# Kernel tuning notes

Hardware: AMD Instinct MI355X
Metric: run time of the kernel (lower is better)

The kernel has to match this reference:

```python
import jax, jax.numpy as jnp
import numpy as np

NU, NI, E, D = 100000, 50000, 500000, 64
L = 3  # number of NGCF layers
SLOPE = 0.2
EPS = 1e-12


def setup_inputs() -> dict:
    key = jax.random.key(0)
    ks = jax.random.split(key, 12)
    scale = 1.0 / np.sqrt(D)  # roughly xavier-ish magnitude
    return {
        "feat_user": jax.random.normal(ks[0], (NU, D), jnp.float32) * scale,
        "feat_item": jax.random.normal(ks[1], (NI, D), jnp.float32) * scale,
        "W1": jax.random.normal(ks[2], (L, D, D), jnp.float32) * scale,
        "b1": jnp.zeros((L, D), jnp.float32),
        "W2": jax.random.normal(ks[3], (L, D, D), jnp.float32) * scale,
        "b2": jnp.zeros((L, D), jnp.float32),
        "u_idx": jax.random.randint(ks[4], (E,), 0, NU),
        "i_idx": jax.random.randint(ks[5], (E,), 0, NI),
        "users": jax.random.randint(ks[6], (8192,), 0, NU),
        "pos_items": jax.random.randint(ks[7], (8192,), 0, NI),
        "neg_items": jax.random.randint(ks[8], (8192,), 0, NI),
    }


def _l2norm(h):
    n = jnp.sqrt(jnp.sum(h * h, axis=1, keepdims=True))
    return h / jnp.maximum(n, EPS)


def reference(feat_user, feat_item, W1, b1, W2, b2, u_idx, i_idx, users, pos_items, neg_items):
    # symmetric edge norm 1/sqrt(deg_u * deg_i), same for both directions
    ones = jnp.ones((E,), jnp.float32)
    deg_u = jax.ops.segment_sum(ones, u_idx, num_segments=NU)
    deg_i = jax.ops.segment_sum(ones, i_idx, num_segments=NI)
    norm = (deg_u[u_idx] * deg_i[i_idx]) ** -0.5  # [E]
    norm = norm[:, None]

    hu, hi = feat_user, feat_item
    user_embeds, item_embeds = [hu], [hi]
    for l in range(L):
        w1, bb1, w2, bb2 = W1[l], b1[l], W2[l], b2[l]
        pu = hu @ w1 + bb1  # self-loop message W1(h) per user node
        pi = hi @ w1 + bb1
        eu = hu[u_idx]      # [E, D] gathered src features
        ei = hi[i_idx]
        pw = (eu * ei) @ w2 + bb2  # shared elementwise-product term
        m_u2i = norm * (pu[u_idx] + pw)  # user -> item messages
        m_i2u = norm * (pi[i_idx] + pw)  # item -> user messages
        hu = pu + jax.ops.segment_sum(m_i2u, u_idx, num_segments=NU)
        hi = pi + jax.ops.segment_sum(m_u2i, i_idx, num_segments=NI)
        hu = _l2norm(jax.nn.leaky_relu(hu, SLOPE))
        hi = _l2norm(jax.nn.leaky_relu(hi, SLOPE))
        user_embeds.append(hu)
        item_embeds.append(hi)

    user_embd = jnp.concatenate(user_embeds, axis=1)  # [NU, (L+1)*D]
    item_embd = jnp.concatenate(item_embeds, axis=1)
    return (user_embd[users], item_embd[pos_items], item_embd[neg_items])
```

## Files before the change

kernel.cpp:

```cpp
#include <hip/hip_runtime.h>

#define NU_N 100000
#define NI_N 50000
#define NN_N 150000
#define E_N  500000
#define NSEL 8192
#define GB   18750
#define OB   1536

typedef short s8v __attribute__((ext_vector_type(8)));
typedef short s4v __attribute__((ext_vector_type(4)));
typedef float f4v __attribute__((ext_vector_type(4)));

__device__ __forceinline__ float bf2f(unsigned short h) {
  union { unsigned u; float f; } v; v.u = ((unsigned)h) << 16; return v.f;
}
__device__ __forceinline__ unsigned short f2bf(float f) {
  union { float f; unsigned u; } v; v.f = f;
  unsigned u = v.u;
  u += 0x7FFFu + ((u >> 16) & 1u);
  return (unsigned short)(u >> 16);
}

__global__ void k_cvtW(const float* __restrict__ w1, const float* __restrict__ w2,
                       unsigned short* __restrict__ o1, unsigned short* __restrict__ o2) {
  int t = blockIdx.x * blockDim.x + threadIdx.x;
  if (t >= 3 * 8 * 64) return;
  int lane = t & 63;
  int fk = (t >> 6) & 7;
  int l = t >> 9;
  int n = fk >> 1, kh = fk & 1;
  int lm = lane & 15, lqq = lane >> 4;
  int dst = l * 4096 + (fk << 9) + (lane << 3);
  s8v v1, v2;
#pragma unroll
  for (int j = 0; j < 8; j++) {
    int src = l * 4096 + (32 * kh + 8 * lqq + j) * 64 + 16 * n + lm;
    v1[j] = (short)f2bf(w1[src]);
    v2[j] = (short)f2bf(w2[src]);
  }
  *(s8v*)(o1 + dst) = v1;
  *(s8v*)(o2 + dst) = v2;
}

__global__ void k_cvt8s(const float* __restrict__ fu, const float* __restrict__ fi,
                        unsigned short* __restrict__ h, unsigned short* __restrict__ hs,
                        const float* __restrict__ rdeg) {
  int t = blockIdx.x * blockDim.x + threadIdx.x;
  if (t >= NN_N * 8) return;
  int i = t * 8;
  int row = t >> 3;
  const float* src = row < NU_N ? (fu + i) : (fi + (i - NU_N * 64));
  float rw = rdeg[row];
  float4 a = *(const float4*)(src);
  float4 b = *(const float4*)(src + 4);
  s8v o, os;
  o[0] = (short)f2bf(a.x); os[0] = (short)f2bf(a.x * rw);
  o[1] = (short)f2bf(a.y); os[1] = (short)f2bf(a.y * rw);
  o[2] = (short)f2bf(a.z); os[2] = (short)f2bf(a.z * rw);
  o[3] = (short)f2bf(a.w); os[3] = (short)f2bf(a.w * rw);
  o[4] = (short)f2bf(b.x); os[4] = (short)f2bf(b.x * rw);
  o[5] = (short)f2bf(b.y); os[5] = (short)f2bf(b.y * rw);
  o[6] = (short)f2bf(b.z); os[6] = (short)f2bf(b.z * rw);
  o[7] = (short)f2bf(b.w); os[7] = (short)f2bf(b.w * rw);
  *(s8v*)(h + i) = o;
  *(s8v*)(hs + i) = os;
}

__global__ void k_build(const int* __restrict__ u_idx, const int* __restrict__ i_idx,
                        int* __restrict__ cnt,
                        unsigned short* __restrict__ nbrU, int* __restrict__ nbrI) {
  int t = blockIdx.x * blockDim.x + threadIdx.x;
  if (t >= E_N / 4) return;
  int e = t * 4;
  int4 uu = *(const int4*)(u_idx + e);
  int4 ii = *(const int4*)(i_idx + e);
  int u[4] = {uu.x, uu.y, uu.z, uu.w};
  int it[4] = {ii.x, ii.y, ii.z, ii.w};
  int su[4], si[4];
#pragma unroll
  for (int k = 0; k < 4; k++) su[k] = atomicAdd(cnt + u[k], 1);
#pragma unroll
  for (int k = 0; k < 4; k++) si[k] = atomicAdd(cnt + NU_N + it[k], 1);
#pragma unroll
  for (int k = 0; k < 4; k++) {
    if (su[k] < 32) nbrU[(u[k] << 5) + su[k]] = (unsigned short)it[k];
    if (si[k] < 64) nbrI[(it[k] << 6) + si[k]] = u[k];
  }
}

__global__ void k_meta(const int* __restrict__ cnt, float* __restrict__ rdeg) {
  int g = blockIdx.x * blockDim.x + threadIdx.x;
  if (g >= NN_N) return;
  int d = cnt[g];
  rdeg[g] = d > 0 ? 1.0f / sqrtf((float)d) : 0.0f;
}

__device__ __forceinline__ void out_body(int t, const float* __restrict__ fu,
                                         const float* __restrict__ fi,
                                         const unsigned short* __restrict__ h,
                                         const int* __restrict__ users,
                                         const int* __restrict__ pos,
                                         const int* __restrict__ neg,
                                         float* __restrict__ out, int l) {
  int j4 = (t & 15) * 4;
  int row = (t >> 4) & (NSEL - 1);
  int grp = t >> 17;
  int sr = grp == 0 ? users[row] : (grp == 1 ? pos[row] : neg[row]);
  float4 v;
  if (l == 0) {
    const float* f = grp == 0 ? fu : fi;
    v = *(const float4*)(f + (size_t)sr * 64 + j4);
  } else {
    const unsigned short* hh = h + (size_t)(grp == 0 ? sr : NU_N + sr) * 64 + j4;
    s4v x = *(const s4v*)hh;
    v.x = bf2f((unsigned short)x[0]); v.y = bf2f((unsigned short)x[1]);
    v.z = bf2f((unsigned short)x[2]); v.w = bf2f((unsigned short)x[3]);
  }
  *(float4*)(out + (size_t)grp * NSEL * 256 + (size_t)row * 256 + (size_t)l * 64 + j4) = v;
}

template <int CSUM>
__global__ void k_gather(const unsigned short* __restrict__ hs,
                         const int* __restrict__ cnt,
                         const unsigned short* __restrict__ nbrU, const int* __restrict__ nbrI,
                         const float* __restrict__ rdeg,
                         unsigned short* __restrict__ s, float* __restrict__ csum,
                         const float* __restrict__ fu, const float* __restrict__ fi,
                         const unsigned short* __restrict__ h,
                         const int* __restrict__ users, const int* __restrict__ pos,
                         const int* __restrict__ neg, float* __restrict__ out, int lslice) {
  if (blockIdx.x >= GB) {
    int t = (blockIdx.x - GB) * 256 + threadIdx.x;
    out_body(t, fu, fi, h, users, pos, neg, out, lslice);
    return;
  }
  int wv = (blockIdx.x * blockDim.x + threadIdx.x) >> 6;
  int lane = threadIdx.x & 63;
  int half = lane >> 5;
  int lane32 = lane & 31;
  int q = lane32 >> 3;
  int m = lane & 7;
  int g = wv * 2 + half;
  int d = cnt[g];
  bool isU = g < NU_N;
  int dcap = isU ? 32 : 64;
  d = d < dcap ? d : dcap;
  int k0 = isU ? (g << 5) : ((g - NU_N) << 6);
  int myid = NN_N;
  if (lane32 < d) myid = isU ? (NU_N + (int)nbrU[k0 + lane32]) : nbrI[k0 + lane32];
  float myw = 0.0f;
  if (CSUM) myw = rdeg[myid];
  float acc[8] = {0.f, 0.f, 0.f, 0.f, 0.f, 0.f, 0.f, 0.f};
  float c = 0.f;
  int dc = d < 32 ? d : 32;
  int nit = (dc + 15) >> 4;
  int nitA = __shfl(nit, 0), nitB = __shfl(nit, 32);
  int niter = nitA > nitB ? nitA : nitB;
  for (int i = 0; i < niter; i++) {
    int b0 = (half << 5) + (i << 4) + q;
    int n0 = __shfl(myid, b0);
    int n1 = __shfl(myid, b0 + 4);
    int n2 = __shfl(myid, b0 + 8);
    int n3 = __shfl(myid, b0 + 12);
    if (CSUM) {
      c += __shfl(myw, b0) + __shfl(myw, b0 + 4) +
           __shfl(myw, b0 + 8) + __shfl(myw, b0 + 12);
    }
    s8v v0 = *(const s8v*)(hs + (size_t)n0 * 64 + m * 8);
    s8v v1 = *(const s8v*)(hs + (size_t)n1 * 64 + m * 8);
    s8v v2 = *(const s8v*)(hs + (size_t)n2 * 64 + m * 8);
    s8v v3 = *(const s8v*)(hs + (size_t)n3 * 64 + m * 8);
#pragma unroll
    for (int j = 0; j < 8; j++)
      acc[j] += (bf2f((unsigned short)v0[j]) + bf2f((unsigned short)v1[j])) +
                (bf2f((unsigned short)v2[j]) + bf2f((unsigned short)v3[j]));
  }
  for (int t = 32 + q; t < d; t += 4) {
    int nb = nbrI[k0 + t];
    if (CSUM) c += rdeg[nb];
    s8v v = *(const s8v*)(hs + (size_t)nb * 64 + m * 8);
#pragma unroll
    for (int j = 0; j < 8; j++) acc[j] += bf2f((unsigned short)v[j]);
  }
#pragma unroll
  for (int off = 8; off <= 16; off <<= 1) {
#pragma unroll
    for (int j = 0; j < 8; j++) acc[j] += __shfl_xor(acc[j], off);
    if (CSUM) c += __shfl_xor(c, off);
  }
  float rw = rdeg[g];
  if (q == 0) {
    s8v ov;
#pragma unroll
    for (int j = 0; j < 8; j++) ov[j] = (short)f2bf(acc[j] * rw);
    *(s8v*)(s + (size_t)g * 64 + m * 8) = ov;
    if (CSUM && m == 0) csum[g] = c;
  }
}

__global__ void k_update(unsigned short* __restrict__ h, unsigned short* __restrict__ hs,
                         const unsigned short* __restrict__ s,
                         const float* __restrict__ csum, const float* __restrict__ rdeg,
                         const unsigned short* __restrict__ w1s, const unsigned short* __restrict__ w2s,
                         const float* __restrict__ b1, const float* __restrict__ b2) {
  int lane = threadIdx.x & 63;
  int lm = lane & 15, lq = lane >> 4;
  int tile = (blockIdx.x * blockDim.x + threadIdx.x) >> 6;
  if (tile >= NN_N / 16) return;
  s8v f1[4][2], f2w[4][2];
#pragma unroll
  for (int n = 0; n < 4; n++)
#pragma unroll
    for (int kh = 0; kh < 2; kh++) {
      int off = (((n << 1) | kh) << 9) + (lane << 3);
      f1[n][kh]  = *(const s8v*)(w1s + off);
      f2w[n][kh] = *(const s8v*)(w2s + off);
    }
  int m0 = tile << 4;
  size_t rowo = (size_t)(m0 + lm) * 64;
  s8v h0 = *(const s8v*)(h + rowo + 8 * lq);
  s8v h1 = *(const s8v*)(h + rowo + 32 + 8 * lq);
  s8v s0 = *(const s8v*)(s + rowo + 8 * lq);
  s8v s1 = *(const s8v*)(s + rowo + 32 + 8 * lq);
  s8v a10, a11, a20, a21;
#pragma unroll
  for (int j = 0; j < 8; j++) {
    float hv0 = bf2f((unsigned short)h0[j]), sv0 = bf2f((unsigned short)s0[j]);
    float hv1 = bf2f((unsigned short)h1[j]), sv1 = bf2f((unsigned short)s1[j]);
    a10[j] = (short)f2bf(hv0 + sv0); a20[j] = (short)f2bf(hv0 * sv0);
    a11[j] = (short)f2bf(hv1 + sv1); a21[j] = (short)f2bf(hv1 * sv1);
  }
  f4v c[4];
#pragma unroll
  for (int n = 0; n < 4; n++) c[n] = (f4v){0.f, 0.f, 0.f, 0.f};
#pragma unroll
  for (int n = 0; n < 4; n++) {
    c[n] = __builtin_amdgcn_mfma_f32_16x16x32_bf16(a10, f1[n][0], c[n], 0, 0, 0);
    c[n] = __builtin_amdgcn_mfma_f32_16x16x32_bf16(a11, f1[n][1], c[n], 0, 0, 0);
    c[n] = __builtin_amdgcn_mfma_f32_16x16x32_bf16(a20, f2w[n][0], c[n], 0, 0, 0);
    c[n] = __builtin_amdgcn_mfma_f32_16x16x32_bf16(a21, f2w[n][1], c[n], 0, 0, 0);
  }
  float b1c[4], b2c[4];
#pragma unroll
  for (int n = 0; n < 4; n++) { b1c[n] = b1[16 * n + lm]; b2c[n] = b2[16 * n + lm]; }
  float cm[4], rd[4];
#pragma unroll
  for (int r = 0; r < 4; r++) {
    int row = m0 + 4 * lq + r;
    rd[r] = rdeg[row];
    cm[r] = csum[row] * rd[r];
  }
  float x[4][4], ss[4] = {0.f, 0.f, 0.f, 0.f};
#pragma unroll
  for (int n = 0; n < 4; n++)
#pragma unroll
    for (int r = 0; r < 4; r++) {
      float v = c[n][r] + b1c[n] + cm[r] * (b1c[n] + b2c[n]);
      v = v > 0.0f ? v : 0.2f * v;
      x[n][r] = v;
      ss[r] += v * v;
    }
#pragma unroll
  for (int r = 0; r < 4; r++) {
#pragma unroll
    for (int off = 1; off < 16; off <<= 1) ss[r] += __shfl_xor(ss[r], off);
    ss[r] = 1.0f / fmaxf(sqrtf(ss[r]), 1e-12f);
  }
#pragma unroll
  for (int n = 0; n < 4; n++)
#pragma unroll
    for (int r = 0; r < 4; r++) {
      size_t o = (size_t)(m0 + 4 * lq + r) * 64 + 16 * n + lm;
      float hv = x[n][r] * ss[r];
      h[o]  = f2bf(hv);
      hs[o] = f2bf(hv * rd[r]);
    }
}

__global__ void k_out(const float* __restrict__ fu, const float* __restrict__ fi,
                      const unsigned short* __restrict__ h,
                      const int* __restrict__ users, const int* __restrict__ pos,
                      const int* __restrict__ neg, float* __restrict__ out, int l) {
  int t = blockIdx.x * blockDim.x + threadIdx.x;
  if (t >= 3 * NSEL * 16) return;
  out_body(t, fu, fi, h, users, pos, neg, out, l);
}

extern "C" void kernel_launch(void* const* d_in, const int* in_sizes, int n_in,
                              void* d_out, int out_size, void* d_ws, size_t ws_size,
                              hipStream_t stream) {
  (void)in_sizes; (void)n_in; (void)out_size; (void)ws_size;
  const float* fu = (const float*)d_in[0];
  const float* fi = (const float*)d_in[1];
  const float* W1 = (const float*)d_in[2];
  const float* b1 = (const float*)d_in[3];
  const float* W2 = (const float*)d_in[4];
  const float* b2 = (const float*)d_in[5];
  const int* u_idx = (const int*)d_in[6];
  const int* i_idx = (const int*)d_in[7];
  const int* users = (const int*)d_in[8];
  const int* pos   = (const int*)d_in[9];
  const int* neg   = (const int*)d_in[10];
  float* out = (float*)d_out;

  char* w = (char*)d_ws;
  auto alloc = [&](size_t bytes) { char* p = w; w += (bytes + 255) & ~(size_t)255; return p; };
  unsigned short* h  = (unsigned short*)alloc((size_t)NN_N * 64 * 2);
  unsigned short* hs = (unsigned short*)alloc((size_t)(NN_N + 1) * 64 * 2);
  unsigned short* sb = (unsigned short*)alloc((size_t)NN_N * 64 * 2);
  int*   cnt  = (int*)alloc((size_t)NN_N * 4);
  float* csum = (float*)alloc((size_t)NN_N * 4);
  float* rdeg = (float*)alloc((size_t)(NN_N + 1) * 4);
  unsigned short* nbrU = (unsigned short*)alloc((size_t)NU_N * 32 * 2);
  int*   nbrI = (int*)alloc((size_t)NI_N * 64 * 4);
  unsigned short* w1s = (unsigned short*)alloc((size_t)3 * 4096 * 2);
  unsigned short* w2s = (unsigned short*)alloc((size_t)3 * 4096 * 2);

  hipMemsetAsync(cnt, 0, (size_t)NN_N * 4, stream);
  hipMemsetAsync(hs + (size_t)NN_N * 64, 0, 128, stream);
  hipMemsetAsync(rdeg + NN_N, 0, 4, stream);
  k_build<<<(E_N / 4 + 255) / 256, 256, 0, stream>>>(u_idx, i_idx, cnt, nbrU, nbrI);
  k_meta<<<(NN_N + 255) / 256, 256, 0, stream>>>(cnt, rdeg);

  k_cvt8s<<<(NN_N * 8 + 255) / 256, 256, 0, stream>>>(fu, fi, h, hs, rdeg);
  k_cvtW<<<(3 * 8 * 64 + 255) / 256, 256, 0, stream>>>(W1, W2, w1s, w2s);

  for (int l = 0; l < 3; l++) {
    if (l == 0)
      k_gather<1><<<GB + OB, 256, 0, stream>>>(hs, cnt, nbrU, nbrI, rdeg, sb, csum,
                                               fu, fi, h, users, pos, neg, out, 0);
    else
      k_gather<0><<<GB + OB, 256, 0, stream>>>(hs, cnt, nbrU, nbrI, rdeg, sb, csum,
                                               fu, fi, h, users, pos, neg, out, l);
    k_update<<<((NN_N / 16) * 64 + 255) / 256, 256, 0, stream>>>(
        h, hs, sb, csum, rdeg, w1s + (size_t)l * 4096, w2s + (size_t)l * 4096,
        b1 + (size_t)l * 64, b2 + (size_t)l * 64);
  }
  k_out<<<(3 * NSEL * 16 + 255) / 256, 256, 0, stream>>>(fu, fi, h, users, pos, neg, out, 3);
}
```

Before: 228.3 us.

## Drop pre-scaled hs buffer, apply degree weights in gather, fuse init kernels

Removes the separate degree-prescaled bf16 feature copy (hs). The gather now reads h directly and multiplies each neighbour row by its rdeg weight, which it loads anyway. The edge-build, feature-conversion and weight-conversion kernels are merged into one launch. Feature conversion no longer waits for rdeg, so it can overlap with the atomic edge build. The aim is to cut the extra hs write in each update and at init, plus two kernel launches. The cost is extra multiplies in the gather and one fewer rounding step, which changes numerics slightly. The edge build also moves from four edges per thread to one.

```diff
diff --git a/kernel.cpp b/kernel.cpp
--- a/kernel.cpp
+++ b/kernel.cpp
@@ -7,6 +7,9 @@
 #define NSEL 8192
 #define GB   18750
 #define OB   1536
+#define BB   1954
+#define CB   4688
+#define WB   6
 
 typedef short s8v __attribute__((ext_vector_type(8)));
 typedef short s4v __attribute__((ext_vector_type(4)));
@@ -22,70 +25,57 @@
   return (unsigned short)(u >> 16);
 }
 
-__global__ void k_cvtW(const float* __restrict__ w1, const float* __restrict__ w2,
+__global__ void k_init(const int* __restrict__ u_idx, const int* __restrict__ i_idx,
+                       int* __restrict__ cnt,
+                       unsigned short* __restrict__ nbrU, int* __restrict__ nbrI,
+                       const float* __restrict__ fu, const float* __restrict__ fi,
+                       unsigned short* __restrict__ h,
+                       const float* __restrict__ w1, const float* __restrict__ w2,
                        unsigned short* __restrict__ o1, unsigned short* __restrict__ o2) {
-  int t = blockIdx.x * blockDim.x + threadIdx.x;
-  if (t >= 3 * 8 * 64) return;
-  int lane = t & 63;
-  int fk = (t >> 6) & 7;
-  int l = t >> 9;
-  int n = fk >> 1, kh = fk & 1;
-  int lm = lane & 15, lqq = lane >> 4;
-  int dst = l * 4096 + (fk << 9) + (lane << 3);
-  s8v v1, v2;
-#pragma unroll
-  for (int j = 0; j < 8; j++) {
-    int src = l * 4096 + (32 * kh + 8 * lqq + j) * 64 + 16 * n + lm;
-    v1[j] = (short)f2bf(w1[src]);
-    v2[j] = (short)f2bf(w2[src]);
-  }
-  *(s8v*)(o1 + dst) = v1;
-  *(s8v*)(o2 + dst) = v2;
-}
-
-__global__ void k_cvt8s(const float* __restrict__ fu, const float* __restrict__ fi,
-                        unsigned short* __restrict__ h, unsigned short* __restrict__ hs,
-                        const float* __restrict__ rdeg) {
-  int t = blockIdx.x * blockDim.x + threadIdx.x;
-  if (t >= NN_N * 8) return;
-  int i = t * 8;
-  int row = t >> 3;
-  const float* src = row < NU_N ? (fu + i) : (fi + (i - NU_N * 64));
-  float rw = rdeg[row];
-  float4 a = *(const float4*)(src);
-  float4 b = *(const float4*)(src + 4);
-  s8v o, os;
-  o[0] = (short)f2bf(a.x); os[0] = (short)f2bf(a.x * rw);
-  o[1] = (short)f2bf(a.y); os[1] = (short)f2bf(a.y * rw);
-  o[2] = (short)f2bf(a.z); os[2] = (short)f2bf(a.z * rw);
-  o[3] = (short)f2bf(a.w); os[3] = (short)f2bf(a.w * rw);
-  o[4] = (short)f2bf(b.x); os[4] = (short)f2bf(b.x * rw);
-  o[5] = (short)f2bf(b.y); os[5] = (short)f2bf(b.y * rw);
-  o[6] = (short)f2bf(b.z); os[6] = (short)f2bf(b.z * rw);
-  o[7] = (short)f2bf(b.w); os[7] = (short)f2bf(b.w * rw);
-  *(s8v*)(h + i) = o;
-  *(s8v*)(hs + i) = os;
-}
-
-__global__ void k_build(const int* __restrict__ u_idx, const int* __restrict__ i_idx,
-                        int* __restrict__ cnt,
-                        unsigned short* __restrict__ nbrU, int* __restrict__ nbrI) {
-  int t = blockIdx.x * blockDim.x + threadIdx.x;
-  if (t >= E_N / 4) return;
-  int e = t * 4;
-  int4 uu = *(const int4*)(u_idx + e);
-  int4 ii = *(const int4*)(i_idx + e);
-  int u[4] = {uu.x, uu.y, uu.z, uu.w};
-  int it[4] = {ii.x, ii.y, ii.z, ii.w};
-  int su[4], si[4];
-#pragma unroll
-  for (int k = 0; k < 4; k++) su[k] = atomicAdd(cnt + u[k], 1);
-#pragma unroll
-  for (int k = 0; k < 4; k++) si[k] = atomicAdd(cnt + NU_N + it[k], 1);
-#pragma unroll
-  for (int k = 0; k < 4; k++) {
-    if (su[k] < 32) nbrU[(u[k] << 5) + su[k]] = (unsigned short)it[k];
-    if (si[k] < 64) nbrI[(it[k] << 6) + si[k]] = u[k];
+  int b = blockIdx.x;
+  if (b < BB) {
+    int e = b * 256 + threadIdx.x;
+    if (e >= E_N) return;
+    int u = u_idx[e], it = i_idx[e];
+    int su = atomicAdd(cnt + u, 1);
+    if (su < 32) nbrU[(u << 5) + su] = (unsigned short)it;
+    int si = atomicAdd(cnt + NU_N + it, 1);
+    if (si < 64) nbrI[(it << 6) + si] = u;
+    return;
+  }
+  if (b < BB + CB) {
+    int t = (b - BB) * 256 + threadIdx.x;
+    if (t >= NN_N * 8) return;
+    int i = t * 8;
+    const float* src = i < NU_N * 64 ? (fu + i) : (fi + (i - NU_N * 64));
+    float4 a = *(const float4*)(src);
+    float4 bb = *(const float4*)(src + 4);
+    s8v o;
+    o[0] = (short)f2bf(a.x);  o[1] = (short)f2bf(a.y);
+    o[2] = (short)f2bf(a.z);  o[3] = (short)f2bf(a.w);
+    o[4] = (short)f2bf(bb.x); o[5] = (short)f2bf(bb.y);
+    o[6] = (short)f2bf(bb.z); o[7] = (short)f2bf(bb.w);
+    *(s8v*)(h + i) = o;
+    return;
+  }
+  {
+    int t = (b - BB - CB) * 256 + threadIdx.x;
+    if (t >= 3 * 8 * 64) return;
+    int lane = t & 63;
+    int fk = (t >> 6) & 7;
+    int l = t >> 9;
+    int n = fk >> 1, kh = fk & 1;
+    int lm = lane & 15, lqq = lane >> 4;
+    int dst = l * 4096 + (fk << 9) + (lane << 3);
+    s8v v1, v2;
+#pragma unroll
+    for (int j = 0; j < 8; j++) {
+      int src = l * 4096 + (32 * kh + 8 * lqq + j) * 64 + 16 * n + lm;
+      v1[j] = (short)f2bf(w1[src]);
+      v2[j] = (short)f2bf(w2[src]);
+    }
+    *(s8v*)(o1 + dst) = v1;
+    *(s8v*)(o2 + dst) = v2;
   }
 }
 
@@ -121,13 +111,12 @@
 }
 
 template <int CSUM>
-__global__ void k_gather(const unsigned short* __restrict__ hs,
+__global__ void k_gather(const unsigned short* __restrict__ h,
                          const int* __restrict__ cnt,
                          const unsigned short* __restrict__ nbrU, const int* __restrict__ nbrI,
                          const float* __restrict__ rdeg,
                          unsigned short* __restrict__ s, float* __restrict__ csum,
                          const float* __restrict__ fu, const float* __restrict__ fi,
-                         const unsigned short* __restrict__ h,
                          const int* __restrict__ users, const int* __restrict__ pos,
                          const int* __restrict__ neg, float* __restrict__ out, int lslice) {
   if (blockIdx.x >= GB) {
@@ -149,8 +138,7 @@
   int k0 = isU ? (g << 5) : ((g - NU_N) << 6);
   int myid = NN_N;
   if (lane32 < d) myid = isU ? (NU_N + (int)nbrU[k0 + lane32]) : nbrI[k0 + lane32];
-  float myw = 0.0f;
-  if (CSUM) myw = rdeg[myid];
+  float myw = rdeg[myid];
   float acc[8] = {0.f, 0.f, 0.f, 0.f, 0.f, 0.f, 0.f, 0.f};
   float c = 0.f;
   int dc = d < 32 ? d : 32;
@@ -163,25 +151,27 @@
     int n1 = __shfl(myid, b0 + 4);
     int n2 = __shfl(myid, b0 + 8);
     int n3 = __shfl(myid, b0 + 12);
-    if (CSUM) {
-      c += __shfl(myw, b0) + __shfl(myw, b0 + 4) +
-           __shfl(myw, b0 + 8) + __shfl(myw, b0 + 12);
-    }
-    s8v v0 = *(const s8v*)(hs + (size_t)n0 * 64 + m * 8);
-    s8v v1 = *(const s8v*)(hs + (size_t)n1 * 64 + m * 8);
-    s8v v2 = *(const s8v*)(hs + (size_t)n2 * 64 + m * 8);
-    s8v v3 = *(const s8v*)(hs + (size_t)n3 * 64 + m * 8);
+    float w0 = __shfl(myw, b0);
+    float w1 = __shfl(myw, b0 + 4);
+    float w2 = __shfl(myw, b0 + 8);
+    float w3 = __shfl(myw, b0 + 12);
+    if (CSUM) c += (w0 + w1) + (w2 + w3);
+    s8v v0 = *(const s8v*)(h + (size_t)n0 * 64 + m * 8);
+    s8v v1 = *(const s8v*)(h + (size_t)n1 * 64 + m * 8);
+    s8v v2 = *(const s8v*)(h + (size_t)n2 * 64 + m * 8);
+    s8v v3 = *(const s8v*)(h + (size_t)n3 * 64 + m * 8);
 #pragma unroll
     for (int j = 0; j < 8; j++)
-      acc[j] += (bf2f((unsigned short)v0[j]) + bf2f((unsigned short)v1[j])) +
-                (bf2f((unsigned short)v2[j]) + bf2f((unsigned short)v3[j]));
+      acc[j] += (w0 * bf2f((unsigned short)v0[j]) + w1 * bf2f((unsigned short)v1[j])) +
+                (w2 * bf2f((unsigned short)v2[j]) + w3 * bf2f((unsigned short)v3[j]));
   }
   for (int t = 32 + q; t < d; t += 4) {
     int nb = nbrI[k0 + t];
-    if (CSUM) c += rdeg[nb];
-    s8v v = *(const s8v*)(hs + (size_t)nb * 64 + m * 8);
-#pragma unroll
-    for (int j = 0; j < 8; j++) acc[j] += bf2f((unsigned short)v[j]);
+    float w = rdeg[nb];
+    if (CSUM) c += w;
+    s8v v = *(const s8v*)(h + (size_t)nb * 64 + m * 8);
+#pragma unroll
+    for (int j = 0; j < 8; j++) acc[j] += w * bf2f((unsigned short)v[j]);
   }
 #pragma unroll
   for (int off = 8; off <= 16; off <<= 1) {
@@ -199,7 +189,7 @@
   }
 }
 
-__global__ void k_update(unsigned short* __restrict__ h, unsigned short* __restrict__ hs,
+__global__ void k_update(unsigned short* __restrict__ h,
                          const unsigned short* __restrict__ s,
                          const float* __restrict__ csum, const float* __restrict__ rdeg,
                          const unsigned short* __restrict__ w1s, const unsigned short* __restrict__ w2s,
@@ -244,12 +234,11 @@
   float b1c[4], b2c[4];
 #pragma unroll
   for (int n = 0; n < 4; n++) { b1c[n] = b1[16 * n + lm]; b2c[n] = b2[16 * n + lm]; }
-  float cm[4], rd[4];
+  float cm[4];
 #pragma unroll
   for (int r = 0; r < 4; r++) {
     int row = m0 + 4 * lq + r;
-    rd[r] = rdeg[row];
-    cm[r] = csum[row] * rd[r];
+    cm[r] = csum[row] * rdeg[row];
   }
   float x[4][4], ss[4] = {0.f, 0.f, 0.f, 0.f};
 #pragma unroll
@@ -272,9 +261,7 @@
 #pragma unroll
     for (int r = 0; r < 4; r++) {
       size_t o = (size_t)(m0 + 4 * lq + r) * 64 + 16 * n + lm;
-      float hv = x[n][r] * ss[r];
-      h[o]  = f2bf(hv);
-      hs[o] = f2bf(hv * rd[r]);
+      h[o] = f2bf(x[n][r] * ss[r]);
     }
 }
 
@@ -306,8 +293,7 @@
 
   char* w = (char*)d_ws;
   auto alloc = [&](size_t bytes) { char* p = w; w += (bytes + 255) & ~(size_t)255; return p; };
-  unsigned short* h  = (unsigned short*)alloc((size_t)NN_N * 64 * 2);
-  unsigned short* hs = (unsigned short*)alloc((size_t)(NN_N + 1) * 64 * 2);
+  unsigned short* h  = (unsigned short*)alloc((size_t)(NN_N + 1) * 64 * 2);
   unsigned short* sb = (unsigned short*)alloc((size_t)NN_N * 64 * 2);
   int*   cnt  = (int*)alloc((size_t)NN_N * 4);
   float* csum = (float*)alloc((size_t)NN_N * 4);
@@ -318,23 +304,21 @@
   unsigned short* w2s = (unsigned short*)alloc((size_t)3 * 4096 * 2);
 
   hipMemsetAsync(cnt, 0, (size_t)NN_N * 4, stream);
-  hipMemsetAsync(hs + (size_t)NN_N * 64, 0, 128, stream);
+  hipMemsetAsync(h + (size_t)NN_N * 64, 0, 128, stream);
   hipMemsetAsync(rdeg + NN_N, 0, 4, stream);
-  k_build<<<(E_N / 4 + 255) / 256, 256, 0, stream>>>(u_idx, i_idx, cnt, nbrU, nbrI);
+  k_init<<<BB + CB + WB, 256, 0, stream>>>(u_idx, i_idx, cnt, nbrU, nbrI,
+                                           fu, fi, h, W1, W2, w1s, w2s);
   k_meta<<<(NN_N + 255) / 256, 256, 0, stream>>>(cnt, rdeg);
-
-  k_cvt8s<<<(NN_N * 8 + 255) / 256, 256, 0, stream>>>(fu, fi, h, hs, rdeg);
-  k_cvtW<<<(3 * 8 * 64 + 255) / 256, 256, 0, stream>>>(W1, W2, w1s, w2s);
 
   for (int l = 0; l < 3; l++) {
     if (l == 0)
-      k_gather<1><<<GB + OB, 256, 0, stream>>>(hs, cnt, nbrU, nbrI, rdeg, sb, csum,
-                                               fu, fi, h, users, pos, neg, out, 0);
+      k_gather<1><<<GB + OB, 256, 0, stream>>>(h, cnt, nbrU, nbrI, rdeg, sb, csum,
+                                               fu, fi, users, pos, neg, out, 0);
     else
-      k_gather<0><<<GB + OB, 256, 0, stream>>>(hs, cnt, nbrU, nbrI, rdeg, sb, csum,
-                                               fu, fi, h, users, pos, neg, out, l);
+      k_gather<0><<<GB + OB, 256, 0, stream>>>(h, cnt, nbrU, nbrI, rdeg, sb, csum,
+                                               fu, fi, users, pos, neg, out, l);
     k_update<<<((NN_N / 16) * 64 + 255) / 256, 256, 0, stream>>>(
-        h, hs, sb, csum, rdeg, w1s + (size_t)l * 4096, w2s + (size_t)l * 4096,
+        h, sb, csum, rdeg, w1s + (size_t)l * 4096, w2s + (size_t)l * 4096,
         b1 + (size_t)l * 64, b2 + (size_t)l * 64);
   }
   k_out<<<(3 * NSEL * 16 + 255) / 256, 256, 0, stream>>>(fu, fi, h, users, pos, neg, out, 3);
```

New measurement: 244.9 us. 7.3% more time.
